# Optimization experiments

Measured on AMD Instinct MI355X. Metric: run time of the kernel, lower is better.

The kernel has to match this reference:

```python
import jax, jax.numpy as jnp
import numpy as np

NUM_SEGMENTS = 256
HIDDEN = 512
N_NODES = 100000


def setup_inputs() -> dict:
    key = jax.random.key(0)
    k_x, k_b, k_w, k_bias = jax.random.split(key, 4)
    x = jax.random.normal(k_x, (N_NODES, HIDDEN), dtype=jnp.float32)
    batch = jnp.sort(jax.random.randint(k_b, (N_NODES,), 0, NUM_SEGMENTS, dtype=jnp.int64))
    # gate_nn = Linear(hidden_size, 1)
    bound = 1.0 / np.sqrt(HIDDEN)
    W = jax.random.uniform(k_w, (HIDDEN, 1), dtype=jnp.float32, minval=-bound, maxval=bound)
    b = jax.random.uniform(k_bias, (1,), dtype=jnp.float32, minval=-bound, maxval=bound)
    return {"x": x, "batch": batch, "W": W, "b": b}


def reference(x, batch, W, b):
    # gate = gate_nn(x) -> [N, 1]
    gate = (x @ W + b)[:, 0]  # [N]
    # segment-wise numerically-stable softmax over nodes of each graph
    gmax = jax.ops.segment_max(gate, batch, num_segments=NUM_SEGMENTS)  # [B]
    e = jnp.exp(gate - gmax[batch])  # [N]
    denom = jax.ops.segment_sum(e, batch, num_segments=NUM_SEGMENTS)  # [B]
    alpha = e / (denom[batch] + 1e-16)  # [N]
    # weighted scatter-sum pooling: out[b] = sum_{i in b} alpha_i * x_i
    out = jax.ops.segment_sum(alpha[:, None] * x, batch, num_segments=NUM_SEGMENTS)  # [B, H]
    return out
```

## Files before the change

kernel.cpp:

```cpp
#include <hip/hip_runtime.h>

#define N_SEG 256
#define HIDDEN 512
#define CHUNKS 16
#define NEG_INF (-__builtin_inff())

__global__ __launch_bounds__(256) void fused_kernel(
    const float* __restrict__ x, const float* __restrict__ W,
    const int* __restrict__ batch,
    float* __restrict__ pacc, float* __restrict__ pm, float* __restrict__ pd,
    int n) {
    int b = blockIdx.x;
    int s = b >> 4, c = b & 15;
    int t = threadIdx.x, lane = t & 63, w = t >> 6;

    int lo = 0, hi = n;
    while (lo < hi) { int mid = (lo + hi) >> 1; if (batch[mid] < s) lo = mid + 1; else hi = mid; }
    int ss = lo; hi = n;
    while (lo < hi) { int mid = (lo + hi) >> 1; if (batch[mid] < s + 1) lo = mid + 1; else hi = mid; }
    int se = lo;
    int len = se - ss;
    int st = ss + (int)(((long long)len * c) >> 4);
    int en = ss + (int)(((long long)len * (c + 1)) >> 4);

    if (st >= en) {
        if (t == 0) { pm[b] = NEG_INF; pd[b] = 0.0f; }
        for (int j = t; j < HIDDEN; j += 256) pacc[(size_t)b * HIDDEN + j] = 0.0f;
        return;
    }

    float4 w0 = *(const float4*)(W + lane * 8);
    float4 w1 = *(const float4*)(W + lane * 8 + 4);
    float m = NEG_INF, d = 0.0f;
    float acc[8] = {0, 0, 0, 0, 0, 0, 0, 0};

    int i = st + w;
    bool have = i < en;
    float4 a0, a1;
    if (have) {
        const float* xr = x + (size_t)i * HIDDEN + lane * 8;
        a0 = *(const float4*)xr; a1 = *(const float4*)(xr + 4);
    }
    while (have) {
        int inext = i + 4;
        bool hnext = inext < en;
        float4 b0, b1;
        if (hnext) {
            const float* xr = x + (size_t)inext * HIDDEN + lane * 8;
            b0 = *(const float4*)xr; b1 = *(const float4*)(xr + 4);
        }
        float g = a0.x * w0.x + a0.y * w0.y + a0.z * w0.z + a0.w * w0.w
                + a1.x * w1.x + a1.y * w1.y + a1.z * w1.z + a1.w * w1.w;
        #pragma unroll
        for (int off = 32; off; off >>= 1) g += __shfl_xor(g, off, 64);
        float mn = fmaxf(m, g);
        float scale = __expf(m - mn);
        float p = __expf(g - mn);
        d = d * scale + p;
        acc[0] = acc[0] * scale + p * a0.x;  acc[1] = acc[1] * scale + p * a0.y;
        acc[2] = acc[2] * scale + p * a0.z;  acc[3] = acc[3] * scale + p * a0.w;
        acc[4] = acc[4] * scale + p * a1.x;  acc[5] = acc[5] * scale + p * a1.y;
        acc[6] = acc[6] * scale + p * a1.z;  acc[7] = acc[7] * scale + p * a1.w;
        m = mn;
        a0 = b0; a1 = b1; i = inext; have = hnext;
    }

    __shared__ float sm[4], sd[4];
    __shared__ float sacc[4][HIDDEN];
    if (lane == 0) sm[w] = m;
    __syncthreads();
    float M = fmaxf(fmaxf(sm[0], sm[1]), fmaxf(sm[2], sm[3]));
    float scale = (m == NEG_INF) ? 0.0f : __expf(m - M);
    if (lane == 0) sd[w] = d * scale;
    #pragma unroll
    for (int j = 0; j < 8; ++j) sacc[w][lane * 8 + j] = acc[j] * scale;
    __syncthreads();
    if (t == 0) { pm[b] = M; pd[b] = sd[0] + sd[1] + sd[2] + sd[3]; }
    for (int j = t; j < HIDDEN; j += 256)
        pacc[(size_t)b * HIDDEN + j] = sacc[0][j] + sacc[1][j] + sacc[2][j] + sacc[3][j];
}

__global__ __launch_bounds__(256) void merge_kernel(
    const float* __restrict__ pacc, const float* __restrict__ pm,
    const float* __restrict__ pd, float* __restrict__ out) {
    int s = blockIdx.x, t = threadIdx.x;
    int k0 = s * CHUNKS;
    float M = NEG_INF;
    #pragma unroll
    for (int k = 0; k < CHUNKS; ++k) M = fmaxf(M, pm[k0 + k]);
    float wts[CHUNKS];
    float D = 0.0f;
    #pragma unroll
    for (int k = 0; k < CHUNKS; ++k) {
        float mk = pm[k0 + k];
        float wk = (mk == NEG_INF) ? 0.0f : __expf(mk - M);
        wts[k] = wk;
        D += pd[k0 + k] * wk;
    }
    float invD = 1.0f / (D + 1e-16f);
    #pragma unroll
    for (int rep = 0; rep < 2; ++rep) {
        int col = t + rep * 256;
        float num = 0.0f;
        #pragma unroll
        for (int k = 0; k < CHUNKS; ++k)
            num += pacc[(size_t)(k0 + k) * HIDDEN + col] * wts[k];
        out[s * HIDDEN + col] = num * invD;
    }
}

extern "C" void kernel_launch(void* const* d_in, const int* in_sizes, int n_in,
                              void* d_out, int out_size, void* d_ws, size_t ws_size,
                              hipStream_t stream) {
    const float* x     = (const float*)d_in[0];
    const int*   batch = (const int*)d_in[1];
    const float* W     = (const float*)d_in[2];
    int n = in_sizes[1];
    float* out = (float*)d_out;

    const int nb = N_SEG * CHUNKS;
    float* pacc = (float*)d_ws;
    float* pm   = pacc + (size_t)nb * HIDDEN;
    float* pd   = pm + nb;

    fused_kernel<<<nb, 256, 0, stream>>>(x, W, batch, pacc, pm, pd, n);
    merge_kernel<<<N_SEG, 256, 0, stream>>>(pacc, pm, pd, out);
}
```

Baseline: 48.10 us.

## Partition rows evenly across blocks instead of per-segment chunks

The fused kernel now splits the node rows into 2048 equal contiguous ranges and processes every segment run inside its range, writing partial softmax state into slots indexed by each run's start row. The binary search for segment bounds moves to the merge kernel, which gathers only the partials that overlap its segment. This is meant to balance load across blocks and remove the per-block binary searches and empty chunks. In exchange it adds extra syncs per segment boundary, and it needs a workspace sized by n rows and assumes at most 96 rows per block.

```diff
diff --git a/kernel.cpp b/kernel.cpp
--- a/kernel.cpp
+++ b/kernel.cpp
@@ -2,7 +2,9 @@
 
 #define N_SEG 256
 #define HIDDEN 512
-#define CHUNKS 16
+#define NB 2048
+#define NB_SHIFT 11
+#define MAXROWS 96
 #define NEG_INF (-__builtin_inff())
 
 __global__ __launch_bounds__(256) void fused_kernel(
@@ -11,102 +13,128 @@
     float* __restrict__ pacc, float* __restrict__ pm, float* __restrict__ pd,
     int n) {
     int b = blockIdx.x;
-    int s = b >> 4, c = b & 15;
+    int r0 = (int)(((long long)n * b) >> NB_SHIFT);
+    int r1 = (int)(((long long)n * (b + 1)) >> NB_SHIFT);
+    int len = r1 - r0;
     int t = threadIdx.x, lane = t & 63, w = t >> 6;
 
+    float4 pa0, pa1;
+    if (r0 + w < r1) {
+        const float* xr = x + (size_t)(r0 + w) * HIDDEN + lane * 8;
+        pa0 = *(const float4*)xr; pa1 = *(const float4*)(xr + 4);
+    }
+    float4 w0 = *(const float4*)(W + lane * 8);
+    float4 w1 = *(const float4*)(W + lane * 8 + 4);
+
+    __shared__ int sbatch[MAXROWS];
+    if (t < len) sbatch[t] = batch[r0 + t];
+    __syncthreads();
+
+    __shared__ float sm[4], sd[4];
+    __shared__ float sacc[4][HIDDEN];
+
+    int q0 = 0;
+    while (q0 < len) {
+        int seg = sbatch[q0];
+        int q1 = q0 + 1;
+        while (q1 < len && sbatch[q1] == seg) ++q1;
+        int st = r0 + q0, en = r0 + q1;
+
+        float m = NEG_INF, d = 0.0f;
+        float acc[8] = {0, 0, 0, 0, 0, 0, 0, 0};
+        int i = st + w;
+        bool have = i < en;
+        float4 a0, a1;
+        if (have) {
+            if (q0 == 0) { a0 = pa0; a1 = pa1; }
+            else {
+                const float* xr = x + (size_t)i * HIDDEN + lane * 8;
+                a0 = *(const float4*)xr; a1 = *(const float4*)(xr + 4);
+            }
+        }
+        while (have) {
+            int inext = i + 4;
+            bool hnext = inext < en;
+            float4 b0, b1;
+            if (hnext) {
+                const float* xr = x + (size_t)inext * HIDDEN + lane * 8;
+                b0 = *(const float4*)xr; b1 = *(const float4*)(xr + 4);
+            }
+            float g = a0.x * w0.x + a0.y * w0.y + a0.z * w0.z + a0.w * w0.w
+                    + a1.x * w1.x + a1.y * w1.y + a1.z * w1.z + a1.w * w1.w;
+            #pragma unroll
+            for (int off = 32; off; off >>= 1) g += __shfl_xor(g, off, 64);
+            float mn = fmaxf(m, g);
+            float scale = __expf(m - mn);
+            float p = __expf(g - mn);
+            d = d * scale + p;
+            acc[0] = acc[0] * scale + p * a0.x;  acc[1] = acc[1] * scale + p * a0.y;
+            acc[2] = acc[2] * scale + p * a0.z;  acc[3] = acc[3] * scale + p * a0.w;
+            acc[4] = acc[4] * scale + p * a1.x;  acc[5] = acc[5] * scale + p * a1.y;
+            acc[6] = acc[6] * scale + p * a1.z;  acc[7] = acc[7] * scale + p * a1.w;
+            m = mn;
+            a0 = b0; a1 = b1; i = inext; have = hnext;
+        }
+
+        if (lane == 0) sm[w] = m;
+        __syncthreads();
+        float M = fmaxf(fmaxf(sm[0], sm[1]), fmaxf(sm[2], sm[3]));
+        float scale = (m == NEG_INF) ? 0.0f : __expf(m - M);
+        if (lane == 0) sd[w] = d * scale;
+        #pragma unroll
+        for (int j = 0; j < 8; ++j) sacc[w][lane * 8 + j] = acc[j] * scale;
+        __syncthreads();
+        if (t == 0) { pm[st] = M; pd[st] = sd[0] + sd[1] + sd[2] + sd[3]; }
+        for (int j = t; j < HIDDEN; j += 256)
+            pacc[(size_t)st * HIDDEN + j] = sacc[0][j] + sacc[1][j] + sacc[2][j] + sacc[3][j];
+        __syncthreads();
+        q0 = q1;
+    }
+}
+
+__device__ __forceinline__ int b_of(int r, int n) {
+    int b = (int)(((long long)r << NB_SHIFT) / n);
+    while ((int)(((long long)n * (b + 1)) >> NB_SHIFT) <= r) ++b;
+    while ((int)(((long long)n * b) >> NB_SHIFT) > r) --b;
+    return b;
+}
+
+__global__ __launch_bounds__(256) void merge_kernel(
+    const int* __restrict__ batch, const float* __restrict__ pacc,
+    const float* __restrict__ pm, const float* __restrict__ pd,
+    float* __restrict__ out, int n) {
+    int s = blockIdx.x, t = threadIdx.x;
     int lo = 0, hi = n;
     while (lo < hi) { int mid = (lo + hi) >> 1; if (batch[mid] < s) lo = mid + 1; else hi = mid; }
     int ss = lo; hi = n;
     while (lo < hi) { int mid = (lo + hi) >> 1; if (batch[mid] < s + 1) lo = mid + 1; else hi = mid; }
     int se = lo;
-    int len = se - ss;
-    int st = ss + (int)(((long long)len * c) >> 4);
-    int en = ss + (int)(((long long)len * (c + 1)) >> 4);
+    if (ss >= se) { out[s * HIDDEN + t] = 0.0f; out[s * HIDDEN + 256 + t] = 0.0f; return; }
 
-    if (st >= en) {
-        if (t == 0) { pm[b] = NEG_INF; pd[b] = 0.0f; }
-        for (int j = t; j < HIDDEN; j += 256) pacc[(size_t)b * HIDDEN + j] = 0.0f;
-        return;
+    int blo = b_of(ss, n), bhi = b_of(se - 1, n);
+    float M = NEG_INF;
+    for (int b = blo; b <= bhi; ++b) {
+        int r0b = (int)(((long long)n * b) >> NB_SHIFT);
+        int slot = ss > r0b ? ss : r0b;
+        M = fmaxf(M, pm[slot]);
     }
-
-    float4 w0 = *(const float4*)(W + lane * 8);
-    float4 w1 = *(const float4*)(W + lane * 8 + 4);
-    float m = NEG_INF, d = 0.0f;
-    float acc[8] = {0, 0, 0, 0, 0, 0, 0, 0};
-
-    int i = st + w;
-    bool have = i < en;
-    float4 a0, a1;
-    if (have) {
-        const float* xr = x + (size_t)i * HIDDEN + lane * 8;
-        a0 = *(const float4*)xr; a1 = *(const float4*)(xr + 4);
-    }
-    while (have) {
-        int inext = i + 4;
-        bool hnext = inext < en;
-        float4 b0, b1;
-        if (hnext) {
-            const float* xr = x + (size_t)inext * HIDDEN + lane * 8;
-            b0 = *(const float4*)xr; b1 = *(const float4*)(xr + 4);
-        }
-        float g = a0.x * w0.x + a0.y * w0.y + a0.z * w0.z + a0.w * w0.w
-                + a1.x * w1.x + a1.y * w1.y + a1.z * w1.z + a1.w * w1.w;
-        #pragma unroll
-        for (int off = 32; off; off >>= 1) g += __shfl_xor(g, off, 64);
-        float mn = fmaxf(m, g);
-        float scale = __expf(m - mn);
-        float p = __expf(g - mn);
-        d = d * scale + p;
-        acc[0] = acc[0] * scale + p * a0.x;  acc[1] = acc[1] * scale + p * a0.y;
-        acc[2] = acc[2] * scale + p * a0.z;  acc[3] = acc[3] * scale + p * a0.w;
-        acc[4] = acc[4] * scale + p * a1.x;  acc[5] = acc[5] * scale + p * a1.y;
-        acc[6] = acc[6] * scale + p * a1.z;  acc[7] = acc[7] * scale + p * a1.w;
-        m = mn;
-        a0 = b0; a1 = b1; i = inext; have = hnext;
-    }
-
-    __shared__ float sm[4], sd[4];
-    __shared__ float sacc[4][HIDDEN];
-    if (lane == 0) sm[w] = m;
-    __syncthreads();
-    float M = fmaxf(fmaxf(sm[0], sm[1]), fmaxf(sm[2], sm[3]));
-    float scale = (m == NEG_INF) ? 0.0f : __expf(m - M);
-    if (lane == 0) sd[w] = d * scale;
-    #pragma unroll
-    for (int j = 0; j < 8; ++j) sacc[w][lane * 8 + j] = acc[j] * scale;
-    __syncthreads();
-    if (t == 0) { pm[b] = M; pd[b] = sd[0] + sd[1] + sd[2] + sd[3]; }
-    for (int j = t; j < HIDDEN; j += 256)
-        pacc[(size_t)b * HIDDEN + j] = sacc[0][j] + sacc[1][j] + sacc[2][j] + sacc[3][j];
-}
-
-__global__ __launch_bounds__(256) void merge_kernel(
-    const float* __restrict__ pacc, const float* __restrict__ pm,
-    const float* __restrict__ pd, float* __restrict__ out) {
-    int s = blockIdx.x, t = threadIdx.x;
-    int k0 = s * CHUNKS;
-    float M = NEG_INF;
-    #pragma unroll
-    for (int k = 0; k < CHUNKS; ++k) M = fmaxf(M, pm[k0 + k]);
-    float wts[CHUNKS];
     float D = 0.0f;
-    #pragma unroll
-    for (int k = 0; k < CHUNKS; ++k) {
-        float mk = pm[k0 + k];
-        float wk = (mk == NEG_INF) ? 0.0f : __expf(mk - M);
-        wts[k] = wk;
-        D += pd[k0 + k] * wk;
+    for (int b = blo; b <= bhi; ++b) {
+        int r0b = (int)(((long long)n * b) >> NB_SHIFT);
+        int slot = ss > r0b ? ss : r0b;
+        D += pd[slot] * __expf(pm[slot] - M);
     }
     float invD = 1.0f / (D + 1e-16f);
-    #pragma unroll
-    for (int rep = 0; rep < 2; ++rep) {
-        int col = t + rep * 256;
-        float num = 0.0f;
-        #pragma unroll
-        for (int k = 0; k < CHUNKS; ++k)
-            num += pacc[(size_t)(k0 + k) * HIDDEN + col] * wts[k];
-        out[s * HIDDEN + col] = num * invD;
+    float num0 = 0.0f, num1 = 0.0f;
+    for (int b = blo; b <= bhi; ++b) {
+        int r0b = (int)(((long long)n * b) >> NB_SHIFT);
+        int slot = ss > r0b ? ss : r0b;
+        float wt = __expf(pm[slot] - M);
+        num0 += pacc[(size_t)slot * HIDDEN + t] * wt;
+        num1 += pacc[(size_t)slot * HIDDEN + 256 + t] * wt;
     }
+    out[s * HIDDEN + t] = num0 * invD;
+    out[s * HIDDEN + 256 + t] = num1 * invD;
 }
 
 extern "C" void kernel_launch(void* const* d_in, const int* in_sizes, int n_in,
@@ -118,11 +146,10 @@
     int n = in_sizes[1];
     float* out = (float*)d_out;
 
-    const int nb = N_SEG * CHUNKS;
     float* pacc = (float*)d_ws;
-    float* pm   = pacc + (size_t)nb * HIDDEN;
-    float* pd   = pm + nb;
+    float* pm   = pacc + (size_t)n * HIDDEN;
+    float* pd   = pm + n;
 
-    fused_kernel<<<nb, 256, 0, stream>>>(x, W, batch, pacc, pm, pd, n);
-    merge_kernel<<<N_SEG, 256, 0, stream>>>(pacc, pm, pd, out);
+    fused_kernel<<<NB, 256, 0, stream>>>(x, W, batch, pacc, pm, pd, n);
+    merge_kernel<<<N_SEG, 256, 0, stream>>>(batch, pacc, pm, pd, out, n);
 }
```

After: 59.60 us. +23.9%, slower.
